# Kernel tuning notes

Hardware: AMD Instinct MI355X
Metric: run time of the kernel (lower is better)

## Reference

```python
import jax, jax.numpy as jnp
import numpy as np

NUM_CLASSES = 91
COST_CLASS, COST_BBOX, COST_GIOU = 1.0, 5.0, 2.0
W_CE, W_BBOX, W_GIOU = 2.0, 2.5, 2.0
EOS_COEF = 0.1
B, Q, T = 64, 300, 25


def box_cxcywh_to_xyxy(x):
    cx, cy, w, h = x[..., 0], x[..., 1], x[..., 2], x[..., 3]
    return jnp.stack([cx - 0.5 * w, cy - 0.5 * h, cx + 0.5 * w, cy + 0.5 * h], axis=-1)


def giou_pairwise(b1, b2):
    # b1 [N,4], b2 [M,4] in xyxy -> [N,M]
    area1 = (b1[:, 2] - b1[:, 0]) * (b1[:, 3] - b1[:, 1])
    area2 = (b2[:, 2] - b2[:, 0]) * (b2[:, 3] - b2[:, 1])
    lt = jnp.maximum(b1[:, None, :2], b2[None, :, :2])
    rb = jnp.minimum(b1[:, None, 2:], b2[None, :, 2:])
    wh = jnp.clip(rb - lt, 0.0)
    inter = wh[..., 0] * wh[..., 1]
    union = area1[:, None] + area2[None, :] - inter
    iou = inter / union
    lti = jnp.minimum(b1[:, None, :2], b2[None, :, :2])
    rbi = jnp.maximum(b1[:, None, 2:], b2[None, :, 2:])
    whi = jnp.clip(rbi - lti, 0.0)
    areai = whi[..., 0] * whi[..., 1]
    return iou - (areai - union) / areai


def giou_elementwise(b1, b2):
    # b1,b2 [N,4] xyxy -> [N]
    area1 = (b1[:, 2] - b1[:, 0]) * (b1[:, 3] - b1[:, 1])
    area2 = (b2[:, 2] - b2[:, 0]) * (b2[:, 3] - b2[:, 1])
    lt = jnp.maximum(b1[:, :2], b2[:, :2])
    rb = jnp.minimum(b1[:, 2:], b2[:, 2:])
    wh = jnp.clip(rb - lt, 0.0)
    inter = wh[:, 0] * wh[:, 1]
    union = area1 + area2 - inter
    iou = inter / union
    lti = jnp.minimum(b1[:, :2], b2[:, :2])
    rbi = jnp.maximum(b1[:, 2:], b2[:, 2:])
    whi = jnp.clip(rbi - lti, 0.0)
    areai = whi[:, 0] * whi[:, 1]
    return iou - (areai - union) / areai


def _lsa(cost):
    # Jonker-Volgenant shortest augmenting path; same optimum as scipy linear_sum_assignment
    cost = np.asarray(cost, dtype=np.float64)
    transposed = cost.shape[0] > cost.shape[1]
    if transposed:
        cost = cost.T
    n, m = cost.shape  # n <= m
    u = np.zeros(n + 1)
    v = np.zeros(m + 1)
    p = np.zeros(m + 1, dtype=np.int64)
    way = np.zeros(m + 1, dtype=np.int64)
    for i in range(1, n + 1):
        p[0] = i
        j0 = 0
        minv = np.full(m + 1, np.inf)
        used = np.zeros(m + 1, dtype=bool)
        while True:
            used[j0] = True
            i0 = p[j0]
            cur = cost[i0 - 1, :] - u[i0] - v[1:]
            free = ~used[1:]
            better = free & (cur < minv[1:])
            minv[1:][better] = cur[better]
            way[1:][better] = j0
            masked = np.where(free, minv[1:], np.inf)
            j1 = int(np.argmin(masked)) + 1
            delta = minv[j1]
            u[p[used]] += delta
            v[used] -= delta
            minv[~used] -= delta
            j0 = j1
            if p[j0] == 0:
                break
        while j0:
            j1 = way[j0]
            p[j0] = p[j1]
            j0 = j1
    rows, cols = [], []
    for j in range(1, m + 1):
        if p[j] != 0:
            rows.append(p[j] - 1)
            cols.append(j - 1)
    rows = np.asarray(rows, dtype=np.int64)
    cols = np.asarray(cols, dtype=np.int64)
    if transposed:
        rows, cols = cols, rows
    order = np.argsort(rows)
    return rows[order], cols[order]


def _match(pred_logits, pred_boxes, tgt_labels, tgt_boxes):
    # builds the full cross-batch cost matrix exactly like the torch module, then
    # solves per-image rectangular assignment on the host (non-differentiable)
    log_prob = jax.nn.log_softmax(pred_logits.reshape(B * Q, NUM_CLASSES + 1), axis=-1)
    out_bbox = pred_boxes.reshape(B * Q, 4)
    tgt_ids = tgt_labels.reshape(B * T)
    tgt_bb = tgt_boxes.reshape(B * T, 4)
    cost_class = -log_prob[:, tgt_ids]                                        # [BQ, BT]
    cost_bbox = jnp.abs(out_bbox[:, None, :] - tgt_bb[None, :, :]).sum(-1)    # L1 cdist
    cost_giou = -giou_pairwise(box_cxcywh_to_xyxy(out_bbox), box_cxcywh_to_xyxy(tgt_bb))
    C = COST_BBOX * cost_bbox + COST_CLASS * cost_class + COST_GIOU * cost_giou
    Cn = np.asarray(jax.lax.stop_gradient(C.reshape(B, Q, B * T)))
    src = np.zeros((B, T), dtype=np.int64)
    tgt = np.zeros((B, T), dtype=np.int64)
    for b in range(B):
        r, c = _lsa(Cn[b, :, b * T:(b + 1) * T])
        src[b] = r
        tgt[b] = c
    batch_idx = jnp.repeat(jnp.arange(B), T)
    return batch_idx, jnp.asarray(src.reshape(-1)), jnp.asarray(tgt.reshape(-1))


def _losses(pred_logits, pred_boxes, tgt_labels, tgt_boxes, batch_idx, src_idx, tgt_idx):
    num_t = batch_idx.shape[0]
    matched_labels = tgt_labels[batch_idx, tgt_idx]
    target_classes = jnp.full((B, Q), NUM_CLASSES, dtype=jnp.int32)
    target_classes = target_classes.at[batch_idx, src_idx].set(matched_labels)
    empty_weight = jnp.ones(NUM_CLASSES + 1, dtype=pred_logits.dtype).at[-1].set(EOS_COEF)
    logp = jax.nn.log_softmax(pred_logits, axis=-1)
    nll = -jnp.take_along_axis(logp, target_classes[..., None], axis=-1)[..., 0]
    w = empty_weight[target_classes]
    loss_ce = (w * nll).sum() / w.sum()
    src_b = pred_boxes[batch_idx, src_idx]
    tgt_b = tgt_boxes[batch_idx, tgt_idx]
    loss_bbox = jnp.abs(src_b - tgt_b).sum() / num_t
    loss_giou = (1.0 - giou_elementwise(box_cxcywh_to_xyxy(src_b), box_cxcywh_to_xyxy(tgt_b))).sum() / num_t
    l_ce = W_CE * loss_ce
    l_bb = W_BBOX * loss_bbox
    l_gi = W_GIOU * loss_giou
    return jnp.stack([l_ce, l_bb, l_gi, l_ce + l_bb + l_gi])


def setup_inputs() -> dict:
    key = jax.random.key(0)
    k1, k2, k3, k4 = jax.random.split(key, 4)
    pred_logits = jax.random.normal(k1, (B, Q, NUM_CLASSES + 1), dtype=jnp.float32)
    pred_boxes = jax.random.uniform(k2, (B, Q, 4), dtype=jnp.float32, minval=0.05, maxval=0.95)
    tgt_labels = jax.random.randint(k3, (B, T), 0, NUM_CLASSES)
    tgt_boxes = jax.random.uniform(k4, (B, T, 4), dtype=jnp.float32, minval=0.05, maxval=0.95)
    return {"pred_logits": pred_logits, "pred_boxes": pred_boxes, "tgt_labels": tgt_labels, "tgt_boxes": tgt_boxes}


def reference(pred_logits, pred_boxes, tgt_labels, tgt_boxes):
    batch_idx, src_idx, tgt_idx = _match(pred_logits, pred_boxes, tgt_labels, tgt_boxes)
    # returns [loss_ce, loss_bbox, loss_giou, loss_total] (already weight-scaled)
    return _losses(pred_logits, pred_boxes, tgt_labels, tgt_boxes, batch_idx, src_idx, tgt_idx)
```

## Files before the change

### kernel.cpp

```cpp
#include <hip/hip_runtime.h>
#include <math.h>

constexpr int B_ = 64;
constexpr int Q_ = 300;
constexpr int T_ = 25;
constexpr int NCLS = 91;
constexpr int L_ = NCLS + 1;
constexpr float C_BB = 5.0f, C_GI = 2.0f;
constexpr float W_CE = 2.0f, W_BBOX = 2.5f, W_GIOU = 2.0f;
constexpr float EOS = 0.1f;
constexpr int K_ = 5;
constexpr int TPB = 256;

__device__ __forceinline__ unsigned long long packkey(double v, int j, int p) {
    long long bb = __double_as_longlong(v);
    unsigned long long u = (bb < 0) ? ~(unsigned long long)bb
                                    : ((unsigned long long)bb | 0x8000000000000000ULL);
    return (u & ~16383ULL) | ((unsigned long long)(unsigned)j << 5)
                           | (unsigned long long)(unsigned)p;
}
__device__ __forceinline__ double unpackkey(unsigned long long key) {
    unsigned long long u = key & ~16383ULL;
    unsigned long long bb = (u & 0x8000000000000000ULL) ? (u & 0x7FFFFFFFFFFFFFFFULL)
                                                        : ~u;
    return __longlong_as_double((long long)bb);
}
__device__ __forceinline__ unsigned int ord32(float f) {
    unsigned int b = __float_as_uint(f);
    return (b & 0x80000000u) ? ~b : (b | 0x80000000u);
}
__device__ __forceinline__ float unord32(unsigned int o) {
    unsigned int b = (o & 0x80000000u) ? (o & 0x7FFFFFFFu) : ~o;
    return __uint_as_float(b);
}

template <int CTRL>
__device__ __forceinline__ unsigned long long dppmin(unsigned long long b) {
    int lo = __builtin_amdgcn_update_dpp(0, (int)(unsigned)b, CTRL, 0xF, 0xF, true);
    int hi = __builtin_amdgcn_update_dpp(0, (int)(unsigned)(b >> 32), CTRL, 0xF, 0xF, true);
    unsigned long long o = ((unsigned long long)(unsigned)hi << 32) | (unsigned)lo;
    return o < b ? o : b;
}
__device__ __forceinline__ unsigned long long swz16min(unsigned long long b) {
    int lo = __builtin_amdgcn_ds_swizzle((int)(unsigned)b, 0x401F);
    int hi = __builtin_amdgcn_ds_swizzle((int)(unsigned)(b >> 32), 0x401F);
    unsigned long long o = ((unsigned long long)(unsigned)hi << 32) | (unsigned)lo;
    return o < b ? o : b;
}

__device__ __forceinline__ float giou_f(const float px[4], float parea,
                                        const float tx[4], float tarea) {
    float ltx = fmaxf(px[0], tx[0]), lty = fmaxf(px[1], tx[1]);
    float rbx = fminf(px[2], tx[2]), rby = fminf(px[3], tx[3]);
    float iw = fmaxf(rbx - ltx, 0.f), ih = fmaxf(rby - lty, 0.f);
    float inter = iw * ih;
    float uni = parea + tarea - inter;
    float iou = inter / uni;
    float lix = fminf(px[0], tx[0]), liy = fminf(px[1], tx[1]);
    float rix = fmaxf(px[2], tx[2]), riy = fmaxf(px[3], tx[3]);
    float aw = fmaxf(rix - lix, 0.f), ah = fmaxf(riy - liy, 0.f);
    float ai = aw * ah;
    return iou - (ai - uni) / ai;
}

__global__ __launch_bounds__(TPB) void fused_kernel(
        const float* __restrict__ logits,
        const float* __restrict__ pboxes,
        const int*   __restrict__ tlabels,
        const float* __restrict__ tboxes,
        double* __restrict__ partial) {
    const int b = blockIdx.x;
    const int tid = threadIdx.x;

    __shared__ float  costL[T_][Q_];
    __shared__ float  lseL[Q_];
    __shared__ unsigned long long keysL[T_][TPB + 1];
    __shared__ unsigned long long key2L[T_][8];
    __shared__ int    pL[Q_ + 1];
    __shared__ int    wayL[Q_ + 1];
    __shared__ double uL[T_ + 1];
    __shared__ int    argcolL[T_];
    __shared__ int    mqL[T_];
    __shared__ int    lblL[T_];
    __shared__ int    lblq[Q_];
    __shared__ float  tbL[T_][4];
    __shared__ float  txL[T_][4];
    __shared__ float  taL[T_];
    __shared__ double wsum[4][3];

    if (tid < T_) {
        lblL[tid] = tlabels[b * T_ + tid];
        float c0 = tboxes[(size_t)(b * T_ + tid) * 4 + 0];
        float c1 = tboxes[(size_t)(b * T_ + tid) * 4 + 1];
        float c2 = tboxes[(size_t)(b * T_ + tid) * 4 + 2];
        float c3 = tboxes[(size_t)(b * T_ + tid) * 4 + 3];
        tbL[tid][0] = c0; tbL[tid][1] = c1; tbL[tid][2] = c2; tbL[tid][3] = c3;
        float x0 = c0 - 0.5f * c2, y0 = c1 - 0.5f * c3;
        float x1 = c0 + 0.5f * c2, y1 = c1 + 0.5f * c3;
        txL[tid][0] = x0; txL[tid][1] = y0; txL[tid][2] = x1; txL[tid][3] = y1;
        taL[tid] = (x1 - x0) * (y1 - y0);
    }
    for (int j = tid; j <= Q_; j += TPB) { pL[j] = 0; wayL[j] = 0; }
    for (int q = tid; q < Q_; q += TPB) lblq[q] = NCLS;
    __syncthreads();

    const float* lgb = logits + (size_t)b * Q_ * L_;
    const float* pbb = pboxes + (size_t)b * Q_ * 4;

    unsigned long long key[T_];
#pragma unroll
    for (int t = 0; t < T_; ++t) key[t] = ~0ULL;

    for (int q = tid; q < Q_; q += TPB) {
        const float4* lr4 = (const float4*)(lgb + (size_t)q * L_);
        float m0 = -INFINITY, m1 = -INFINITY, m2 = -INFINITY, m3 = -INFINITY;
        for (int c = 0; c < 23; ++c) {
            float4 v = lr4[c];
            m0 = fmaxf(m0, v.x); m1 = fmaxf(m1, v.y);
            m2 = fmaxf(m2, v.z); m3 = fmaxf(m3, v.w);
        }
        float mx = fmaxf(fmaxf(m0, m1), fmaxf(m2, m3));
        float s0 = 0.f, s1 = 0.f, s2 = 0.f, s3 = 0.f;
        for (int c = 0; c < 23; ++c) {
            float4 v = lr4[c];
            s0 += expf(v.x - mx); s1 += expf(v.y - mx);
            s2 += expf(v.z - mx); s3 += expf(v.w - mx);
        }
        float lz = mx + logf((s0 + s1) + (s2 + s3));
        lseL[q] = lz;

        float p0 = pbb[(size_t)q * 4 + 0], p1 = pbb[(size_t)q * 4 + 1];
        float p2 = pbb[(size_t)q * 4 + 2], p3 = pbb[(size_t)q * 4 + 3];
        float px[4] = { p0 - 0.5f * p2, p1 - 0.5f * p3, p0 + 0.5f * p2, p1 + 0.5f * p3 };
        float parea = (px[2] - px[0]) * (px[3] - px[1]);

#pragma unroll
        for (int t = 0; t < T_; ++t) {
            float cls = lz - lgb[(size_t)q * L_ + lblL[t]];
            float l1 = fabsf(p0 - tbL[t][0]) + fabsf(p1 - tbL[t][1]) +
                       fabsf(p2 - tbL[t][2]) + fabsf(p3 - tbL[t][3]);
            float tx[4] = { txL[t][0], txL[t][1], txL[t][2], txL[t][3] };
            float g = giou_f(px, parea, tx, taL[t]);
            float cost = C_BB * l1 + cls - C_GI * g;
            costL[t][q] = cost;
            unsigned long long kq =
                ((unsigned long long)ord32(cost) << 32) | (unsigned)q;
            if (kq < key[t]) key[t] = kq;
        }
    }
#pragma unroll
    for (int t = 0; t < T_; ++t) keysL[t][tid] = key[t];
    __syncthreads();

    if (tid < 200) {
        int row = tid >> 3, c = tid & 7;
        unsigned long long best = ~0ULL;
        for (int j = 0; j < 32; ++j) {
            unsigned long long k = keysL[row][c * 32 + j];
            if (k < best) best = k;
        }
        key2L[row][c] = best;
    }
    __syncthreads();

    if (tid < 64) {
        if (tid < T_) {
            unsigned long long rk = ~0ULL;
#pragma unroll
            for (int j = 0; j < 8; ++j) {
                unsigned long long k = key2L[tid][j];
                if (k < rk) rk = k;
            }
            argcolL[tid] = (int)(rk & 0xFFFFFFFFULL);
            uL[tid + 1] = (double)unord32((unsigned)(rk >> 32));
        }
        int win = tid;
        if (tid < T_) {
            int myc = argcolL[tid];
            for (int j = 0; j < T_; ++j) {
                int oc = argcolL[j];
                if (oc == myc && j < win) win = j;
            }
            if (win == tid) pL[myc + 1] = tid + 1;
        }
        unsigned long long matchmask = __ballot(tid < T_ && win == tid);

        double v0[K_], minv[K_], stampv[K_];
        int pReg[K_];
        bool usedk[K_], validk[K_];
#pragma unroll
        for (int k = 0; k < K_; ++k) {
            int col = tid + 64 * k;
            validk[k] = col < Q_;
            v0[k] = 0.0; stampv[k] = 0.0; usedk[k] = false; minv[k] = INFINITY;
            pReg[k] = validk[k] ? pL[col + 1] : 0;
        }

        for (int i = 1; i <= T_; ++i) {
            if (matchmask & (1ULL << (i - 1))) continue;
            if (tid == 0) pL[0] = i;
#pragma unroll
            for (int k = 0; k < K_; ++k) { minv[k] = INFINITY; usedk[k] = false; }
            double S = 0.0;
            int j0 = 0, i0 = i;
            double u0i0 = uL[i];

            for (int step = 0; step < 512; ++step) {
                double a = u0i0 - S;
                const float* crow = &costL[i0 - 1][0];
#pragma unroll
                for (int k = 0; k < K_; ++k) {
                    if (validk[k] && !usedk[k]) {
                        int col = tid + 64 * k;
                        double cur = (double)crow[col] - a - v0[k];
                        if (cur < minv[k]) { minv[k] = cur; wayL[col + 1] = j0; }
                    }
                }
                unsigned long long best = ~0ULL;
#pragma unroll
                for (int k = 0; k < K_; ++k) {
                    if (validk[k] && !usedk[k]) {
                        unsigned long long pk =
                            packkey(minv[k], tid + 1 + 64 * k, pReg[k]);
                        if (pk < best) best = pk;
                    }
                }
                { unsigned long long o = __shfl_xor(best, 32); if (o < best) best = o; }
                best = swz16min(best);
                best = dppmin<0x140>(best);
                best = dppmin<0x141>(best);
                best = dppmin<0x4E>(best);
                best = dppmin<0xB1>(best);

                int j1  = (int)((best >> 5) & 511ULL);
                int i0n = (int)(best & 31ULL);
                double Snew = unpackkey(best);
                S = Snew;
                j0 = j1;
                if (i0n == 0) break;
                int owner = (j1 - 1) & 63, k1 = (j1 - 1) >> 6;
                if (tid == owner) {
#pragma unroll
                    for (int k = 0; k < K_; ++k)
                        if (k == k1) { usedk[k] = true; stampv[k] = Snew; }
                }
                i0 = i0n;
                u0i0 = uL[i0];
            }

#pragma unroll
            for (int k = 0; k < K_; ++k) {
                if (validk[k] && usedk[k]) {
                    double d = S - stampv[k];
                    v0[k] -= d;
                    uL[pReg[k]] += d;
                }
            }
            if (tid == 0) {
                uL[i] += S;
                int jj = j0;
                while (jj) { int jn = wayL[jj]; pL[jj] = pL[jn]; jj = jn; }
            }
#pragma unroll
            for (int k = 0; k < K_; ++k)
                if (validk[k]) pReg[k] = pL[tid + 1 + 64 * k];
        }

#pragma unroll
        for (int k = 0; k < K_; ++k)
            if (validk[k] && pReg[k] > 0) mqL[pReg[k] - 1] = tid + 64 * k;
        if (tid < T_) lblq[mqL[tid]] = lblL[tid];
    }
    __syncthreads();

    double ce = 0.0, sb = 0.0, sg = 0.0;
    for (int q = tid; q < Q_; q += TPB) {
        int label = lblq[q];
        float nll = lseL[q] - lgb[(size_t)q * L_ + label];
        float w = (label == NCLS) ? EOS : 1.0f;
        ce += (double)(w * nll);
    }
    if (tid < T_) {
        int q = mqL[tid];
        float p0 = pbb[(size_t)q * 4 + 0], p1 = pbb[(size_t)q * 4 + 1];
        float p2 = pbb[(size_t)q * 4 + 2], p3 = pbb[(size_t)q * 4 + 3];
        sb = (double)(fabsf(p0 - tbL[tid][0]) + fabsf(p1 - tbL[tid][1]) +
                      fabsf(p2 - tbL[tid][2]) + fabsf(p3 - tbL[tid][3]));
        float px[4] = { p0 - 0.5f * p2, p1 - 0.5f * p3, p0 + 0.5f * p2, p1 + 0.5f * p3 };
        float parea = (px[2] - px[0]) * (px[3] - px[1]);
        float tx[4] = { txL[tid][0], txL[tid][1], txL[tid][2], txL[tid][3] };
        float g = giou_f(px, parea, tx, taL[tid]);
        sg = (double)(1.0f - g);
    }
#pragma unroll
    for (int off = 1; off < 64; off <<= 1) {
        ce += __shfl_xor(ce, off);
        sb += __shfl_xor(sb, off);
        sg += __shfl_xor(sg, off);
    }
    if ((tid & 63) == 0) {
        int w = tid >> 6;
        wsum[w][0] = ce; wsum[w][1] = sb; wsum[w][2] = sg;
    }
    __syncthreads();
    if (tid == 0) {
        double a0 = 0, a1 = 0, a2 = 0;
        for (int w = 0; w < 4; ++w) { a0 += wsum[w][0]; a1 += wsum[w][1]; a2 += wsum[w][2]; }
        partial[(size_t)b * 3 + 0] = a0;
        partial[(size_t)b * 3 + 1] = a1;
        partial[(size_t)b * 3 + 2] = a2;
    }
}

__global__ __launch_bounds__(64) void finalize_kernel(const double* __restrict__ partial,
                                                      float* __restrict__ out) {
    int tid = threadIdx.x;
    double a = partial[(size_t)tid * 3 + 0];
    double c = partial[(size_t)tid * 3 + 1];
    double g = partial[(size_t)tid * 3 + 2];
#pragma unroll
    for (int off = 1; off < 64; off <<= 1) {
        a += __shfl_xor(a, off);
        c += __shfl_xor(c, off);
        g += __shfl_xor(g, off);
    }
    if (tid == 0) {
        float lce = W_CE * (float)(a / 3360.0);
        float lbb = W_BBOX * (float)(c / 1600.0);
        float lgi = W_GIOU * (float)(g / 1600.0);
        out[0] = lce;
        out[1] = lbb;
        out[2] = lgi;
        out[3] = lce + lbb + lgi;
    }
}

extern "C" void kernel_launch(void* const* d_in, const int* in_sizes, int n_in,
                              void* d_out, int out_size, void* d_ws, size_t ws_size,
                              hipStream_t stream) {
    (void)in_sizes; (void)n_in; (void)out_size; (void)ws_size;
    const float* logits  = (const float*)d_in[0];
    const float* pboxes  = (const float*)d_in[1];
    const int*   tlabels = (const int*)d_in[2];
    const float* tboxes  = (const float*)d_in[3];
    float* out = (float*)d_out;
    double* partial = (double*)d_ws;

    fused_kernel<<<B_, TPB, 0, stream>>>(logits, pboxes, tlabels, tboxes, partial);
    finalize_kernel<<<1, 64, 0, stream>>>(partial, out);
}
```

Measured before the change: 36.24 us.

## Add auction-style row reduction and exact 64-bit keys to Hungarian solver

```diff
diff --git a/kernel.cpp b/kernel.cpp
--- a/kernel.cpp
+++ b/kernel.cpp
@@ -12,40 +12,19 @@
 constexpr int K_ = 5;
 constexpr int TPB = 256;
 
-__device__ __forceinline__ unsigned long long packkey(double v, int j, int p) {
+__device__ __forceinline__ unsigned long long ord64(double v) {
     long long bb = __double_as_longlong(v);
-    unsigned long long u = (bb < 0) ? ~(unsigned long long)bb
-                                    : ((unsigned long long)bb | 0x8000000000000000ULL);
-    return (u & ~16383ULL) | ((unsigned long long)(unsigned)j << 5)
-                           | (unsigned long long)(unsigned)p;
-}
-__device__ __forceinline__ double unpackkey(unsigned long long key) {
-    unsigned long long u = key & ~16383ULL;
-    unsigned long long bb = (u & 0x8000000000000000ULL) ? (u & 0x7FFFFFFFFFFFFFFFULL)
-                                                        : ~u;
-    return __longlong_as_double((long long)bb);
+    return (bb < 0) ? ~(unsigned long long)bb
+                    : ((unsigned long long)bb | 0x8000000000000000ULL);
+}
+__device__ __forceinline__ double unord64(unsigned long long u) {
+    long long bb = (u & 0x8000000000000000ULL) ? (long long)(u & 0x7FFFFFFFFFFFFFFFULL)
+                                               : (long long)~u;
+    return __longlong_as_double(bb);
 }
 __device__ __forceinline__ unsigned int ord32(float f) {
     unsigned int b = __float_as_uint(f);
     return (b & 0x80000000u) ? ~b : (b | 0x80000000u);
-}
-__device__ __forceinline__ float unord32(unsigned int o) {
-    unsigned int b = (o & 0x80000000u) ? (o & 0x7FFFFFFFu) : ~o;
-    return __uint_as_float(b);
-}
-
-template <int CTRL>
-__device__ __forceinline__ unsigned long long dppmin(unsigned long long b) {
-    int lo = __builtin_amdgcn_update_dpp(0, (int)(unsigned)b, CTRL, 0xF, 0xF, true);
-    int hi = __builtin_amdgcn_update_dpp(0, (int)(unsigned)(b >> 32), CTRL, 0xF, 0xF, true);
-    unsigned long long o = ((unsigned long long)(unsigned)hi << 32) | (unsigned)lo;
-    return o < b ? o : b;
-}
-__device__ __forceinline__ unsigned long long swz16min(unsigned long long b) {
-    int lo = __builtin_amdgcn_ds_swizzle((int)(unsigned)b, 0x401F);
-    int hi = __builtin_amdgcn_ds_swizzle((int)(unsigned)(b >> 32), 0x401F);
-    unsigned long long o = ((unsigned long long)(unsigned)hi << 32) | (unsigned)lo;
-    return o < b ? o : b;
 }
 
 __device__ __forceinline__ float giou_f(const float px[4], float parea,
@@ -74,8 +53,6 @@
 
     __shared__ float  costL[T_][Q_];
     __shared__ float  lseL[Q_];
-    __shared__ unsigned long long keysL[T_][TPB + 1];
-    __shared__ unsigned long long key2L[T_][8];
     __shared__ int    pL[Q_ + 1];
     __shared__ int    wayL[Q_ + 1];
     __shared__ double uL[T_ + 1];
@@ -90,6 +67,7 @@
 
     if (tid < T_) {
         lblL[tid] = tlabels[b * T_ + tid];
+        mqL[tid] = 0;
         float c0 = tboxes[(size_t)(b * T_ + tid) * 4 + 0];
         float c1 = tboxes[(size_t)(b * T_ + tid) * 4 + 1];
         float c2 = tboxes[(size_t)(b * T_ + tid) * 4 + 2];
@@ -107,10 +85,6 @@
     const float* lgb = logits + (size_t)b * Q_ * L_;
     const float* pbb = pboxes + (size_t)b * Q_ * 4;
 
-    unsigned long long key[T_];
-#pragma unroll
-    for (int t = 0; t < T_; ++t) key[t] = ~0ULL;
-
     for (int q = tid; q < Q_; q += TPB) {
         const float4* lr4 = (const float4*)(lgb + (size_t)q * L_);
         float m0 = -INFINITY, m1 = -INFINITY, m2 = -INFINITY, m3 = -INFINITY;
@@ -141,39 +115,39 @@
                        fabsf(p2 - tbL[t][2]) + fabsf(p3 - tbL[t][3]);
             float tx[4] = { txL[t][0], txL[t][1], txL[t][2], txL[t][3] };
             float g = giou_f(px, parea, tx, taL[t]);
-            float cost = C_BB * l1 + cls - C_GI * g;
-            costL[t][q] = cost;
-            unsigned long long kq =
-                ((unsigned long long)ord32(cost) << 32) | (unsigned)q;
-            if (kq < key[t]) key[t] = kq;
-        }
-    }
-#pragma unroll
-    for (int t = 0; t < T_; ++t) keysL[t][tid] = key[t];
-    __syncthreads();
-
-    if (tid < 200) {
-        int row = tid >> 3, c = tid & 7;
-        unsigned long long best = ~0ULL;
-        for (int j = 0; j < 32; ++j) {
-            unsigned long long k = keysL[row][c * 32 + j];
-            if (k < best) best = k;
-        }
-        key2L[row][c] = best;
+            costL[t][q] = C_BB * l1 + cls - C_GI * g;
+        }
+    }
+    __syncthreads();
+
+    {
+        int w = tid >> 6, lane = tid & 63;
+        for (int t = w; t < T_; t += 4) {
+            unsigned long long best = ~0ULL;
+#pragma unroll
+            for (int k = 0; k < K_; ++k) {
+                int col = lane + 64 * k;
+                if (col < Q_) {
+                    unsigned long long kk =
+                        ((unsigned long long)ord32(costL[t][col]) << 32) | (unsigned)col;
+                    if (kk < best) best = kk;
+                }
+            }
+#pragma unroll
+            for (int off = 1; off < 64; off <<= 1) {
+                unsigned long long o = __shfl_xor(best, off);
+                if (o < best) best = o;
+            }
+            if (lane == 0) {
+                int jc = (int)(best & 0xFFFFFFFFULL);
+                argcolL[t] = jc;
+                uL[t + 1] = (double)costL[t][jc];
+            }
+        }
     }
     __syncthreads();
 
     if (tid < 64) {
-        if (tid < T_) {
-            unsigned long long rk = ~0ULL;
-#pragma unroll
-            for (int j = 0; j < 8; ++j) {
-                unsigned long long k = key2L[tid][j];
-                if (k < rk) rk = k;
-            }
-            argcolL[tid] = (int)(rk & 0xFFFFFFFFULL);
-            uL[tid + 1] = (double)unord32((unsigned)(rk >> 32));
-        }
         int win = tid;
         if (tid < T_) {
             int myc = argcolL[tid];
@@ -183,7 +157,8 @@
             }
             if (win == tid) pL[myc + 1] = tid + 1;
         }
-        unsigned long long matchmask = __ballot(tid < T_ && win == tid);
+        unsigned long long mb = __ballot(tid < T_ && win == tid);
+        unsigned int freemask = (~(unsigned int)mb) & ((1u << T_) - 1);
 
         double v0[K_], minv[K_], stampv[K_];
         int pReg[K_];
@@ -192,12 +167,58 @@
         for (int k = 0; k < K_; ++k) {
             int col = tid + 64 * k;
             validk[k] = col < Q_;
-            v0[k] = 0.0; stampv[k] = 0.0; usedk[k] = false; minv[k] = INFINITY;
+            v0[k] = 0.0;
+            stampv[k] = 0.0; usedk[k] = false; minv[k] = INFINITY;
             pReg[k] = validk[k] ? pL[col + 1] : 0;
         }
 
+        for (int iter = 0; iter < 64 && freemask; ++iter) {
+            int t = __builtin_ctz(freemask);
+            freemask &= freemask - 1;
+
+            double am1 = INFINITY, am2 = INFINITY;
+            int aj1 = Q_;
+            const float* crow = &costL[t][0];
+#pragma unroll
+            for (int k = 0; k < K_; ++k) {
+                if (validk[k]) {
+                    int col = tid + 64 * k;
+                    double h = (double)crow[col] - v0[k];
+                    if (h < am1) { am2 = am1; am1 = h; aj1 = col; }
+                    else if (h < am2) { am2 = h; }
+                }
+            }
+#pragma unroll
+            for (int off = 1; off < 64; off <<= 1) {
+                double om1 = __shfl_xor(am1, off);
+                double om2 = __shfl_xor(am2, off);
+                int    oj1 = __shfl_xor(aj1, off);
+                if (om1 < am1 || (om1 == am1 && oj1 < aj1)) {
+                    am2 = fmin(am1, om2); am1 = om1; aj1 = oj1;
+                } else {
+                    am2 = fmin(am2, om1);
+                }
+            }
+            int j1 = aj1;
+            int owner = j1 & 63, k1 = j1 >> 6;
+            int prev = pL[j1 + 1];
+            bool lowered = (am1 < am2);
+            if (tid == owner && lowered) {
+#pragma unroll
+                for (int k = 0; k < K_; ++k)
+                    if (k == k1) v0[k] -= (am2 - am1);
+            }
+            if (tid == owner) {
+#pragma unroll
+                for (int k = 0; k < K_; ++k)
+                    if (k == k1) pReg[k] = t + 1;
+            }
+            if (tid == 0) { pL[j1 + 1] = t + 1; uL[t + 1] = am2; }
+            if (prev) freemask |= 1u << (prev - 1);
+        }
+
         for (int i = 1; i <= T_; ++i) {
-            if (matchmask & (1ULL << (i - 1))) continue;
+            if (!((freemask >> (i - 1)) & 1u)) continue;
             if (tid == 0) pL[0] = i;
 #pragma unroll
             for (int k = 0; k < K_; ++k) { minv[k] = INFINITY; usedk[k] = false; }
@@ -208,33 +229,28 @@
             for (int step = 0; step < 512; ++step) {
                 double a = u0i0 - S;
                 const float* crow = &costL[i0 - 1][0];
+                unsigned long long bk = ~0ULL;
+                unsigned int ba = 0xFFFFFFFFu;
 #pragma unroll
                 for (int k = 0; k < K_; ++k) {
                     if (validk[k] && !usedk[k]) {
                         int col = tid + 64 * k;
                         double cur = (double)crow[col] - a - v0[k];
                         if (cur < minv[k]) { minv[k] = cur; wayL[col + 1] = j0; }
+                        unsigned long long kk = ord64(minv[k]);
+                        unsigned int aux = ((unsigned)(col + 1) << 5) | (unsigned)pReg[k];
+                        if (kk < bk || (kk == bk && aux < ba)) { bk = kk; ba = aux; }
                     }
                 }
-                unsigned long long best = ~0ULL;
-#pragma unroll
-                for (int k = 0; k < K_; ++k) {
-                    if (validk[k] && !usedk[k]) {
-                        unsigned long long pk =
-                            packkey(minv[k], tid + 1 + 64 * k, pReg[k]);
-                        if (pk < best) best = pk;
-                    }
-                }
-                { unsigned long long o = __shfl_xor(best, 32); if (o < best) best = o; }
-                best = swz16min(best);
-                best = dppmin<0x140>(best);
-                best = dppmin<0x141>(best);
-                best = dppmin<0x4E>(best);
-                best = dppmin<0xB1>(best);
-
-                int j1  = (int)((best >> 5) & 511ULL);
-                int i0n = (int)(best & 31ULL);
-                double Snew = unpackkey(best);
+#pragma unroll
+                for (int off = 1; off < 64; off <<= 1) {
+                    unsigned long long ok = __shfl_xor(bk, off);
+                    unsigned int oa = __shfl_xor(ba, off);
+                    if (ok < bk || (ok == bk && oa < ba)) { bk = ok; ba = oa; }
+                }
+                int j1  = (int)(ba >> 5);
+                int i0n = (int)(ba & 31u);
+                double Snew = unord64(bk);
                 S = Snew;
                 j0 = j1;
                 if (i0n == 0) break;
```

Result: slower. 42.43 us (+17.1%).
